# Performance work log

Measured on AMD Instinct MI355X. Metric: run time of the kernel, lower is better.

## Reference

```python
import jax, jax.numpy as jnp
import numpy as np

NUM_GRAPHS = 512
N_NODES = 100000
N_EDGES = 1600000
D_NODE = 128
D_EDGE = 32
D_OUT = 64


def setup_inputs() -> dict:
    key = jax.random.key(0)
    k = jax.random.split(key, 6)
    x = jax.random.normal(k[0], (N_NODES, D_NODE), dtype=jnp.float32)
    edge_index = jax.random.randint(k[1], (2, N_EDGES), 0, N_NODES, dtype=jnp.int64)
    edge_attr = jax.random.normal(k[2], (N_EDGES, D_EDGE), dtype=jnp.float32)
    u = jax.random.normal(k[3], (NUM_GRAPHS, D_OUT), dtype=jnp.float32)
    batch = jnp.sort(jax.random.randint(k[4], (N_NODES,), 0, NUM_GRAPHS, dtype=jnp.int64))
    W = jax.random.normal(k[5], (D_NODE + D_EDGE, D_OUT), dtype=jnp.float32) * 0.05
    b = jnp.full((D_OUT,), 0.01, dtype=jnp.float32)
    return {"x": x, "edge_index": edge_index, "edge_attr": edge_attr, "u": u, "batch": batch, "W": W, "b": b}


def reference(x, edge_index, edge_attr, u, batch, W, b):
    # row, col = edge_index; only col is used
    col = edge_index[1]
    # scatter_add nodes by graph id -> [B, D_NODE]
    node_aggregate = jax.ops.segment_sum(x, batch, num_segments=NUM_GRAPHS)
    # scatter_add edges by graph id of target node -> [B, D_EDGE]
    edge_aggregate = jax.ops.segment_sum(edge_attr, batch[col], num_segments=NUM_GRAPHS)
    out = jnp.concatenate([node_aggregate, edge_aggregate], axis=1)  # [B, 160]
    return out @ W + b  # [B, 64]
```

## Files before the change

kernel.cpp:

```cpp
#include <hip/hip_runtime.h>

#define NUM_GRAPHS 512
#define N_NODES 100000
#define N_EDGES 1600000
#define D_NODE 128
#define D_EDGE 32
#define D_OUT 64

#define NBLK 512
#define EPB (N_EDGES / NBLK)
#define GCAP 5120

__global__ __launch_bounds__(256) void count_kernel(const int* __restrict__ col,
                                                    const int* __restrict__ batch,
                                                    int* __restrict__ eg,
                                                    int* __restrict__ cnt) {
    __shared__ int c[NUM_GRAPHS];
    const int t = threadIdx.x;
    const int b = blockIdx.x;
    c[t] = 0; c[t + 256] = 0;
    __syncthreads();
    const int base = b * EPB;
    #pragma unroll
    for (int k = 0; k < 6; ++k) {
        const int i0 = k * 512 + t, i1 = i0 + 256;
        const int c0 = col[base + i0], c1 = col[base + i1];
        const int g0 = batch[c0], g1 = batch[c1];
        eg[base + i0] = g0; eg[base + i1] = g1;
        atomicAdd(&c[g0], 1); atomicAdd(&c[g1], 1);
    }
    if (t < EPB - 3072) {
        const int i = 3072 + t;
        const int g = batch[col[base + i]];
        eg[base + i] = g;
        atomicAdd(&c[g], 1);
    }
    __syncthreads();
    cnt[b * NUM_GRAPHS + t]       = c[t];
    cnt[b * NUM_GRAPHS + t + 256] = c[t + 256];
}

__global__ __launch_bounds__(NBLK) void scan_kernel(const int* __restrict__ cnt,
                                                    int* __restrict__ pos,
                                                    int* __restrict__ totals) {
    const int g = blockIdx.x;
    const int t = threadIdx.x;
    __shared__ int sc[NBLK];
    const int v = cnt[t * NUM_GRAPHS + g];
    sc[t] = v;
    __syncthreads();
    for (int off = 1; off < NBLK; off <<= 1) {
        const int x = (t >= off) ? sc[t - off] : 0;
        __syncthreads();
        sc[t] += x;
        __syncthreads();
    }
    pos[t * NUM_GRAPHS + g] = g * GCAP + (sc[t] - v);
    if (t == NBLK - 1) totals[g] = sc[t];
}

__global__ __launch_bounds__(256) void place_kernel(const int* __restrict__ eg,
                                                    const int* __restrict__ pos,
                                                    int* __restrict__ bucket) {
    __shared__ int cur[NUM_GRAPHS];
    const int t = threadIdx.x;
    const int b = blockIdx.x;
    cur[t]       = pos[b * NUM_GRAPHS + t];
    cur[t + 256] = pos[b * NUM_GRAPHS + t + 256];
    __syncthreads();
    const int base = b * EPB;
    #pragma unroll
    for (int k = 0; k < 6; ++k) {
        const int i0 = k * 512 + t, i1 = i0 + 256;
        const int g0 = eg[base + i0], g1 = eg[base + i1];
        const int s0 = atomicAdd(&cur[g0], 1);
        const int s1 = atomicAdd(&cur[g1], 1);
        bucket[s0] = base + i0;
        bucket[s1] = base + i1;
    }
    if (t < EPB - 3072) {
        const int i = 3072 + t;
        const int g = eg[base + i];
        bucket[atomicAdd(&cur[g], 1)] = base + i;
    }
}

__global__ __launch_bounds__(512) void fused_kernel(const float* __restrict__ x,
                                                    const int* __restrict__ batch,
                                                    const float* __restrict__ edge_attr,
                                                    const int* __restrict__ totals,
                                                    const int* __restrict__ bucket,
                                                    const float* __restrict__ W,
                                                    const float* __restrict__ bias,
                                                    float* __restrict__ out) {
    const int g = blockIdx.x;
    const int t = threadIdx.x;
    __shared__ int ids[GCAP];
    __shared__ float4 red[512];
    __shared__ float4 red2[64];
    __shared__ __align__(16) float feat[D_NODE + D_EDGE];

    const int ntot = min(totals[g], GCAP);
    for (int i = t; i < ntot; i += 512) ids[i] = bucket[g * GCAP + i];

    int l = 0, r = N_NODES;
    while (l < r) { int m = (l + r) >> 1; if (batch[m] < g) l = m + 1; else r = m; }
    const int lo = l;
    r = N_NODES;
    while (l < r) { int m = (l + r) >> 1; if (batch[m] < g + 1) l = m + 1; else r = m; }
    const int hi = l;

    const float4* x4 = reinterpret_cast<const float4*>(x);
    const int d4 = t & 31, rr = t >> 5;
    float4 a = make_float4(0.f, 0.f, 0.f, 0.f);
    for (int i = lo + rr; i < hi; i += 16) {
        const float4 v = x4[(size_t)i * 32 + d4];
        a.x += v.x; a.y += v.y; a.z += v.z; a.w += v.w;
    }
    red[t] = a;
    __syncthreads();
    if (t < 32) {
        float4 s = red[t];
        #pragma unroll
        for (int p = 1; p < 16; ++p) {
            const float4 v = red[p * 32 + t];
            s.x += v.x; s.y += v.y; s.z += v.z; s.w += v.w;
        }
        reinterpret_cast<float4*>(feat)[t] = s;
    }

    const float4* ea4 = reinterpret_cast<const float4*>(edge_attr);
    const int slot0 = t >> 3, dq = t & 7;
    float4 a0 = make_float4(0.f, 0.f, 0.f, 0.f);
    float4 a1 = make_float4(0.f, 0.f, 0.f, 0.f);
    float4 a2 = make_float4(0.f, 0.f, 0.f, 0.f);
    float4 a3 = make_float4(0.f, 0.f, 0.f, 0.f);
    for (int base = 0; base < ntot; base += 256) {
        const int s0 = base + slot0, s1 = s0 + 64, s2 = s0 + 128, s3 = s0 + 192;
        const int id0 = (s0 < ntot) ? ids[s0] : -1;
        const int id1 = (s1 < ntot) ? ids[s1] : -1;
        const int id2 = (s2 < ntot) ? ids[s2] : -1;
        const int id3 = (s3 < ntot) ? ids[s3] : -1;
        if (id0 >= 0) { const float4 v = ea4[(size_t)id0 * 8 + dq]; a0.x += v.x; a0.y += v.y; a0.z += v.z; a0.w += v.w; }
        if (id1 >= 0) { const float4 v = ea4[(size_t)id1 * 8 + dq]; a1.x += v.x; a1.y += v.y; a1.z += v.z; a1.w += v.w; }
        if (id2 >= 0) { const float4 v = ea4[(size_t)id2 * 8 + dq]; a2.x += v.x; a2.y += v.y; a2.z += v.z; a2.w += v.w; }
        if (id3 >= 0) { const float4 v = ea4[(size_t)id3 * 8 + dq]; a3.x += v.x; a3.y += v.y; a3.z += v.z; a3.w += v.w; }
    }
    a0.x += a1.x + a2.x + a3.x;
    a0.y += a1.y + a2.y + a3.y;
    a0.z += a1.z + a2.z + a3.z;
    a0.w += a1.w + a2.w + a3.w;
    __syncthreads();
    red[t] = a0;
    __syncthreads();
    if (t < 64) {
        const int part = t >> 3, dq2 = t & 7;
        float4 s = make_float4(0.f, 0.f, 0.f, 0.f);
        #pragma unroll
        for (int k = 0; k < 8; ++k) {
            const float4 v = red[(part * 8 + k) * 8 + dq2];
            s.x += v.x; s.y += v.y; s.z += v.z; s.w += v.w;
        }
        red2[t] = s;
    }
    __syncthreads();
    if (t < 8) {
        float4 s = red2[t];
        #pragma unroll
        for (int k = 1; k < 8; ++k) {
            const float4 v = red2[k * 8 + t];
            s.x += v.x; s.y += v.y; s.z += v.z; s.w += v.w;
        }
        reinterpret_cast<float4*>(feat + D_NODE)[t] = s;
    }
    __syncthreads();

    if (t < D_OUT) {
        float o = bias[t];
        #pragma unroll 8
        for (int k = 0; k < D_NODE + D_EDGE; ++k)
            o += feat[k] * W[k * D_OUT + t];
        out[g * D_OUT + t] = o;
    }
}

extern "C" void kernel_launch(void* const* d_in, const int* in_sizes, int n_in,
                              void* d_out, int out_size, void* d_ws, size_t ws_size,
                              hipStream_t stream) {
    const float* x          = (const float*)d_in[0];
    const int*   edge_index = (const int*)d_in[1];
    const float* edge_attr  = (const float*)d_in[2];
    const int*   batch      = (const int*)d_in[4];
    const float* W          = (const float*)d_in[5];
    const float* b          = (const float*)d_in[6];
    float* out = (float*)d_out;

    const int* col = edge_index + N_EDGES;

    int* eg     = (int*)d_ws;
    int* cnt    = eg + N_EDGES;
    int* pos    = cnt + NBLK * NUM_GRAPHS;
    int* totals = pos + NBLK * NUM_GRAPHS;
    int* bucket = totals + NUM_GRAPHS;

    count_kernel<<<NBLK, 256, 0, stream>>>(col, batch, eg, cnt);
    scan_kernel<<<NUM_GRAPHS, NBLK, 0, stream>>>(cnt, pos, totals);
    place_kernel<<<NBLK, 256, 0, stream>>>(eg, pos, bucket);
    fused_kernel<<<NUM_GRAPHS, 512, 0, stream>>>(x, batch, edge_attr, totals, bucket, W, b, out);
}
```

Measured before the change: 89.35 us.

## Fuse count and place into one pass with fixed per-block slots, scan in consumer

Replaces the count/scan/place three-kernel bucketing with a single pass that writes edge ids into fixed 32-slot buckets per (block, graph), and performs the prefix scan inside the consumer kernel via wave shuffles. The consumer block is widened to 1024 threads. This removes two launches and the intermediate eg/pos arrays, at the cost of scattered bucket reads and a hard cap of 32 edges per block-graph pair that silently drops overflow.

Result: slower. 97.93 us (+9.6%).

```diff
diff --git a/kernel.cpp b/kernel.cpp
--- a/kernel.cpp
+++ b/kernel.cpp
@@ -9,99 +9,51 @@
 
 #define NBLK 512
 #define EPB (N_EDGES / NBLK)
+#define SLOTS 32
 #define GCAP 5120
 
-__global__ __launch_bounds__(256) void count_kernel(const int* __restrict__ col,
-                                                    const int* __restrict__ batch,
-                                                    int* __restrict__ eg,
-                                                    int* __restrict__ cnt) {
-    __shared__ int c[NUM_GRAPHS];
-    const int t = threadIdx.x;
-    const int b = blockIdx.x;
-    c[t] = 0; c[t + 256] = 0;
+__global__ __launch_bounds__(512) void count_place_kernel(const int* __restrict__ col,
+                                                          const int* __restrict__ batch,
+                                                          int* __restrict__ cnt,
+                                                          int* __restrict__ bucket) {
+    __shared__ int cur[NUM_GRAPHS];
+    const int t = threadIdx.x, b = blockIdx.x;
+    cur[t] = 0;
     __syncthreads();
     const int base = b * EPB;
     #pragma unroll
-    for (int k = 0; k < 6; ++k) {
-        const int i0 = k * 512 + t, i1 = i0 + 256;
-        const int c0 = col[base + i0], c1 = col[base + i1];
-        const int g0 = batch[c0], g1 = batch[c1];
-        eg[base + i0] = g0; eg[base + i1] = g1;
-        atomicAdd(&c[g0], 1); atomicAdd(&c[g1], 1);
-    }
-    if (t < EPB - 3072) {
-        const int i = 3072 + t;
-        const int g = batch[col[base + i]];
-        eg[base + i] = g;
-        atomicAdd(&c[g], 1);
+    for (int r = 0; r < 7; ++r) {
+        const int i = r * 512 + t;
+        if (i < EPB) {
+            const int e = base + i;
+            const int g = batch[col[e]];
+            const int s = atomicAdd(&cur[g], 1);
+            if (s < SLOTS) bucket[(((size_t)b << 9) + g) * SLOTS + s] = e;
+        }
     }
     __syncthreads();
-    cnt[b * NUM_GRAPHS + t]       = c[t];
-    cnt[b * NUM_GRAPHS + t + 256] = c[t + 256];
+    cnt[b * NUM_GRAPHS + t] = cur[t];
 }
 
-__global__ __launch_bounds__(NBLK) void scan_kernel(const int* __restrict__ cnt,
-                                                    int* __restrict__ pos,
-                                                    int* __restrict__ totals) {
-    const int g = blockIdx.x;
-    const int t = threadIdx.x;
-    __shared__ int sc[NBLK];
-    const int v = cnt[t * NUM_GRAPHS + g];
-    sc[t] = v;
-    __syncthreads();
-    for (int off = 1; off < NBLK; off <<= 1) {
-        const int x = (t >= off) ? sc[t - off] : 0;
-        __syncthreads();
-        sc[t] += x;
-        __syncthreads();
-    }
-    pos[t * NUM_GRAPHS + g] = g * GCAP + (sc[t] - v);
-    if (t == NBLK - 1) totals[g] = sc[t];
-}
-
-__global__ __launch_bounds__(256) void place_kernel(const int* __restrict__ eg,
-                                                    const int* __restrict__ pos,
-                                                    int* __restrict__ bucket) {
-    __shared__ int cur[NUM_GRAPHS];
-    const int t = threadIdx.x;
-    const int b = blockIdx.x;
-    cur[t]       = pos[b * NUM_GRAPHS + t];
-    cur[t + 256] = pos[b * NUM_GRAPHS + t + 256];
-    __syncthreads();
-    const int base = b * EPB;
-    #pragma unroll
-    for (int k = 0; k < 6; ++k) {
-        const int i0 = k * 512 + t, i1 = i0 + 256;
-        const int g0 = eg[base + i0], g1 = eg[base + i1];
-        const int s0 = atomicAdd(&cur[g0], 1);
-        const int s1 = atomicAdd(&cur[g1], 1);
-        bucket[s0] = base + i0;
-        bucket[s1] = base + i1;
-    }
-    if (t < EPB - 3072) {
-        const int i = 3072 + t;
-        const int g = eg[base + i];
-        bucket[atomicAdd(&cur[g], 1)] = base + i;
-    }
-}
-
-__global__ __launch_bounds__(512) void fused_kernel(const float* __restrict__ x,
-                                                    const int* __restrict__ batch,
-                                                    const float* __restrict__ edge_attr,
-                                                    const int* __restrict__ totals,
-                                                    const int* __restrict__ bucket,
-                                                    const float* __restrict__ W,
-                                                    const float* __restrict__ bias,
-                                                    float* __restrict__ out) {
+__global__ __launch_bounds__(1024) void fused_kernel(const float* __restrict__ x,
+                                                     const int* __restrict__ batch,
+                                                     const float* __restrict__ edge_attr,
+                                                     const int* __restrict__ cnt,
+                                                     const int* __restrict__ bucket,
+                                                     const float* __restrict__ W,
+                                                     const float* __restrict__ bias,
+                                                     float* __restrict__ out) {
     const int g = blockIdx.x;
     const int t = threadIdx.x;
     __shared__ int ids[GCAP];
-    __shared__ float4 red[512];
+    __shared__ float4 red[1024];
     __shared__ float4 red2[64];
     __shared__ __align__(16) float feat[D_NODE + D_EDGE];
+    __shared__ int wtot[8], wbase[8], ntot_s;
 
-    const int ntot = min(totals[g], GCAP);
-    for (int i = t; i < ntot; i += 512) ids[i] = bucket[g * GCAP + i];
+    int n = 0;
+    if (t < NBLK) n = cnt[t * NUM_GRAPHS + g];
+    n = min(n, SLOTS);
 
     int l = 0, r = N_NODES;
     while (l < r) { int m = (l + r) >> 1; if (batch[m] < g) l = m + 1; else r = m; }
@@ -113,21 +65,48 @@
     const float4* x4 = reinterpret_cast<const float4*>(x);
     const int d4 = t & 31, rr = t >> 5;
     float4 a = make_float4(0.f, 0.f, 0.f, 0.f);
-    for (int i = lo + rr; i < hi; i += 16) {
+    for (int i = lo + rr; i < hi; i += 32) {
         const float4 v = x4[(size_t)i * 32 + d4];
         a.x += v.x; a.y += v.y; a.z += v.z; a.w += v.w;
     }
     red[t] = a;
+
+    const int lane = t & 63, w = t >> 6;
+    int v = n;
+    #pragma unroll
+    for (int off = 1; off < 64; off <<= 1) {
+        const int u = __shfl_up(v, off, 64);
+        if (lane >= off) v += u;
+    }
+    if (t < NBLK && lane == 63) wtot[w] = v;
     __syncthreads();
+    if (t == 0) {
+        int s = 0;
+        #pragma unroll
+        for (int i2 = 0; i2 < 8; ++i2) { wbase[i2] = s; s += wtot[i2]; }
+        ntot_s = (s > GCAP) ? GCAP : s;
+    }
     if (t < 32) {
         float4 s = red[t];
         #pragma unroll
-        for (int p = 1; p < 16; ++p) {
-            const float4 v = red[p * 32 + t];
-            s.x += v.x; s.y += v.y; s.z += v.z; s.w += v.w;
+        for (int p = 1; p < 32; ++p) {
+            const float4 u = red[p * 32 + t];
+            s.x += u.x; s.y += u.y; s.z += u.z; s.w += u.w;
         }
         reinterpret_cast<float4*>(feat)[t] = s;
     }
+    __syncthreads();
+
+    if (t < NBLK && n > 0) {
+        int p = wbase[w] + (v - n);
+        const int* src = bucket + (((size_t)t << 9) + g) * SLOTS;
+        for (int j = 0; j < n; ++j) {
+            const int q = p + j;
+            if (q < GCAP) ids[q] = src[j];
+        }
+    }
+    __syncthreads();
+    const int ntot = ntot_s;
 
     const float4* ea4 = reinterpret_cast<const float4*>(edge_attr);
     const int slot0 = t >> 3, dq = t & 7;
@@ -135,16 +114,16 @@
     float4 a1 = make_float4(0.f, 0.f, 0.f, 0.f);
     float4 a2 = make_float4(0.f, 0.f, 0.f, 0.f);
     float4 a3 = make_float4(0.f, 0.f, 0.f, 0.f);
-    for (int base = 0; base < ntot; base += 256) {
-        const int s0 = base + slot0, s1 = s0 + 64, s2 = s0 + 128, s3 = s0 + 192;
+    for (int base = 0; base < ntot; base += 512) {
+        const int s0 = base + slot0, s1 = s0 + 128, s2 = s0 + 256, s3 = s0 + 384;
         const int id0 = (s0 < ntot) ? ids[s0] : -1;
         const int id1 = (s1 < ntot) ? ids[s1] : -1;
         const int id2 = (s2 < ntot) ? ids[s2] : -1;
         const int id3 = (s3 < ntot) ? ids[s3] : -1;
-        if (id0 >= 0) { const float4 v = ea4[(size_t)id0 * 8 + dq]; a0.x += v.x; a0.y += v.y; a0.z += v.z; a0.w += v.w; }
-        if (id1 >= 0) { const float4 v = ea4[(size_t)id1 * 8 + dq]; a1.x += v.x; a1.y += v.y; a1.z += v.z; a1.w += v.w; }
-        if (id2 >= 0) { const float4 v = ea4[(size_t)id2 * 8 + dq]; a2.x += v.x; a2.y += v.y; a2.z += v.z; a2.w += v.w; }
-        if (id3 >= 0) { const float4 v = ea4[(size_t)id3 * 8 + dq]; a3.x += v.x; a3.y += v.y; a3.z += v.z; a3.w += v.w; }
+        if (id0 >= 0) { const float4 u = ea4[(size_t)id0 * 8 + dq]; a0.x += u.x; a0.y += u.y; a0.z += u.z; a0.w += u.w; }
+        if (id1 >= 0) { const float4 u = ea4[(size_t)id1 * 8 + dq]; a1.x += u.x; a1.y += u.y; a1.z += u.z; a1.w += u.w; }
+        if (id2 >= 0) { const float4 u = ea4[(size_t)id2 * 8 + dq]; a2.x += u.x; a2.y += u.y; a2.z += u.z; a2.w += u.w; }
+        if (id3 >= 0) { const float4 u = ea4[(size_t)id3 * 8 + dq]; a3.x += u.x; a3.y += u.y; a3.z += u.z; a3.w += u.w; }
     }
     a0.x += a1.x + a2.x + a3.x;
     a0.y += a1.y + a2.y + a3.y;
@@ -157,9 +136,9 @@
         const int part = t >> 3, dq2 = t & 7;
         float4 s = make_float4(0.f, 0.f, 0.f, 0.f);
         #pragma unroll
-        for (int k = 0; k < 8; ++k) {
-            const float4 v = red[(part * 8 + k) * 8 + dq2];
-            s.x += v.x; s.y += v.y; s.z += v.z; s.w += v.w;
+        for (int k = 0; k < 16; ++k) {
+            const float4 u = red[(part * 16 + k) * 8 + dq2];
+            s.x += u.x; s.y += u.y; s.z += u.z; s.w += u.w;
         }
         red2[t] = s;
     }
@@ -168,8 +147,8 @@
         float4 s = red2[t];
         #pragma unroll
         for (int k = 1; k < 8; ++k) {
-            const float4 v = red2[k * 8 + t];
-            s.x += v.x; s.y += v.y; s.z += v.z; s.w += v.w;
+            const float4 u = red2[k * 8 + t];
+            s.x += u.x; s.y += u.y; s.z += u.z; s.w += u.w;
         }
         reinterpret_cast<float4*>(feat + D_NODE)[t] = s;
     }
@@ -197,14 +176,9 @@
 
     const int* col = edge_index + N_EDGES;
 
-    int* eg     = (int*)d_ws;
-    int* cnt    = eg + N_EDGES;
-    int* pos    = cnt + NBLK * NUM_GRAPHS;
-    int* totals = pos + NBLK * NUM_GRAPHS;
-    int* bucket = totals + NUM_GRAPHS;
+    int* cnt    = (int*)d_ws;
+    int* bucket = cnt + NBLK * NUM_GRAPHS;
 
-    count_kernel<<<NBLK, 256, 0, stream>>>(col, batch, eg, cnt);
-    scan_kernel<<<NUM_GRAPHS, NBLK, 0, stream>>>(cnt, pos, totals);
-    place_kernel<<<NBLK, 256, 0, stream>>>(eg, pos, bucket);
-    fused_kernel<<<NUM_GRAPHS, 512, 0, stream>>>(x, batch, edge_attr, totals, bucket, W, b, out);
+    count_place_kernel<<<NBLK, 512, 0, stream>>>(col, batch, cnt, bucket);
+    fused_kernel<<<NUM_GRAPHS, 1024, 0, stream>>>(x, batch, edge_attr, cnt, bucket, W, b, out);
 }
```
